# Kernel tuning notes

Hardware: AMD Instinct MI355X
Metric: run time of the kernel (lower is better)

Reference implementation:

```python
import jax, jax.numpy as jnp
import numpy as np

N_TAPS = 2
N_DELAY = 1
N_ITER = 3
EPS_MODEL = 1e-5   # LaplaceModel clamp eps (eps_models['laplace'])
EPS = 1e-3         # ISS divide/clamp eps


def mag_sq(x):
    return jnp.real(x) ** 2 + jnp.imag(x) ** 2


def laplace_weights(X):
    # Laplace source model: w[..., c, n] = 1 / (2 * ||X[..., c, :, n]||_2), broadcast over freq
    # X: (..., c, f, n) complex -> weights: (..., c, 1, n) real
    denom = 2.0 * jnp.sqrt(jnp.sum(mag_sq(X), axis=-2, keepdims=True))
    return 1.0 / jnp.maximum(denom, EPS_MODEL)


def iss_type1(src, Xc, weights):
    # Equation (9): update vector for source `src`
    Xs = Xc[..., src, :, :]  # (..., f, n)
    v_num = jnp.mean(weights * Xc * jnp.conj(Xs)[..., None, :, :], axis=-1)  # (..., c, f)
    v_denom = jnp.mean(weights * mag_sq(Xs)[..., None, :, :], axis=-1)       # (..., c, f) real
    v = v_num / jnp.maximum(v_denom, EPS)
    v_s = 1.0 - 1.0 / jnp.sqrt(jnp.maximum(v_denom[..., src, :], EPS))
    v = v.at[..., src, :].set(v_s.astype(v.dtype))
    return v


def iss_type2(src, tap, Xc, X_bar, weights):
    # update vector for dereverberation tap (src, tap)
    Xst = X_bar[..., src, :, tap, :]  # (..., f, n)
    v_num = jnp.mean(weights * Xc * jnp.conj(Xst)[..., None, :, :], axis=-1)
    # NOTE: the source code does NOT apply the 1/n_frames norm to v_denom here
    v_denom = jnp.sum(weights * mag_sq(Xst)[..., None, :, :], axis=-1)
    return v_num / jnp.maximum(v_denom, EPS)


def epoch_update(Xloc, Xc, W, X_bar, n_chan):
    weights = laplace_weights(Xloc)  # (..., c, 1, n)
    g = jnp.maximum(jnp.mean(mag_sq(Xloc), axis=(-2, -1), keepdims=True), 1e-5)
    Xloc = Xloc / jnp.sqrt(g)
    weights = weights * g
    for src in range(n_chan):
        v = iss_type1(src, Xc, weights)  # (..., c, f)
        Xc = Xc - v[..., None] * Xc[..., src, :, :][..., None, :, :]
        W = W - v[..., None] * W[..., src, :, :][..., None, :, :]
    for src in range(n_chan):
        for tap in range(N_TAPS):
            v = iss_type2(src, tap, Xc, X_bar, weights)
            Xc = Xc - v[..., None] * X_bar[..., src, :, tap, :][..., None, :, :]
    return Xloc, Xc, W


def auxiva_t_iss(X):
    batch = X.shape[:-3]
    n_chan, n_freq, n_frames = X.shape[-3:]
    T, D = N_TAPS, N_DELAY
    # hankel view of left-padded signal; keep only the T oldest rows (delayed taps)
    X_pad = jnp.pad(X, [(0, 0)] * (X.ndim - 1) + [(T + D, 0)])
    # X_bar: (..., c, f, T, n), X_bar[..., tap, t] = X[..., t - (T + D) + tap]
    X_bar = jnp.stack([X_pad[..., t:t + n_frames] for t in range(T)], axis=-2)
    eye = jnp.eye(n_chan, dtype=X.dtype)
    W = jnp.broadcast_to(eye[:, None, :], batch + (n_chan, n_freq, n_chan))
    Xloc = X  # the (buggy-but-faithful) local X that only gets renormalized each epoch
    Xc = X    # self.X, the demixed signal updated by ISS
    for _ in range(N_ITER):
        Xloc, Xc, W = epoch_update(Xloc, Xc, W, X_bar, n_chan)
    # projection back: a_f = (W_f^T)^{-1} e1 per frequency
    WT = jnp.swapaxes(jnp.swapaxes(W, -3, -2), -2, -1)  # (..., f, c, c)
    e1 = jnp.zeros((n_chan, 1), dtype=X.dtype).at[0, 0].set(1.0)
    a = jnp.linalg.solve(WT, e1)       # (..., f, c, 1)
    a = jnp.swapaxes(a, -3, -2)        # (..., c, f, 1)
    return Xc * a


def setup_inputs() -> dict:
    key = jax.random.key(0)
    k1, k2 = jax.random.split(key)
    shape = (4, 4, 257, 1024)  # (batch, n_chan, n_freq, n_frames)
    X_real = jax.random.normal(k1, shape, dtype=jnp.float32)
    X_imag = jax.random.normal(k2, shape, dtype=jnp.float32)
    return {"X_real": X_real, "X_imag": X_imag}


def reference(X_real, X_imag):
    X = jax.lax.complex(X_real, X_imag)
    return auxiva_t_iss(X)
```

## Files before the change

kernel.cpp:

```cpp
#include <hip/hip_runtime.h>
#include <math.h>

#define NB 4
#define NC 4
#define NF 257
#define NFR 1024
#define NTOT (NB * NC * NF * NFR)
#define NBC (NB * NC)
#define EPSV 1e-3f
#define EPS_MODEL 1e-5f
#define NCHUNK 32

typedef float v2f __attribute__((ext_vector_type(2)));

__device__ float g_Spart[NCHUNK * NBC * NFR];
__device__ float g_S[NBC * NFR];
__device__ float g_gP[96];

__device__ __forceinline__ float dpp_red_sum(float v) {
  v += __int_as_float(__builtin_amdgcn_update_dpp(0, __float_as_int(v), 0x111, 0xf, 0xf, true));
  v += __int_as_float(__builtin_amdgcn_update_dpp(0, __float_as_int(v), 0x112, 0xf, 0xf, true));
  v += __int_as_float(__builtin_amdgcn_update_dpp(0, __float_as_int(v), 0x114, 0xf, 0xf, true));
  v += __int_as_float(__builtin_amdgcn_update_dpp(0, __float_as_int(v), 0x118, 0xf, 0xf, true));
  v += __int_as_float(__builtin_amdgcn_update_dpp(0, __float_as_int(v), 0x142, 0xa, 0xf, true));
  v += __int_as_float(__builtin_amdgcn_update_dpp(0, __float_as_int(v), 0x143, 0xc, 0xf, true));
  return v;
}

__global__ __launch_bounds__(256) void k_colsum(const float* __restrict__ Xr,
                                                const float* __restrict__ Xi) {
  int u = blockIdx.x * 256 + threadIdx.x;
  int fc = blockIdx.y;
  int f0 = fc * 9;
  int f1 = f0 + 9; if (f1 > NF) f1 = NF;
  int bc = u >> 8, q = u & 255;
  float4 s = make_float4(0.f, 0.f, 0.f, 0.f);
  for (int f = f0; f < f1; ++f) {
    float4 a = reinterpret_cast<const float4*>(Xr + (bc * NF + f) * NFR)[q];
    float4 b = reinterpret_cast<const float4*>(Xi + (bc * NF + f) * NFR)[q];
    s.x += a.x * a.x + b.x * b.x;
    s.y += a.y * a.y + b.y * b.y;
    s.z += a.z * a.z + b.z * b.z;
    s.w += a.w * a.w + b.w * b.w;
  }
  reinterpret_cast<float4*>(g_Spart + fc * (NBC * NFR) + bc * NFR)[q] = s;
}

__global__ __launch_bounds__(256) void k_redgp() {
  int bc = blockIdx.x, tid = threadIdx.x;
  float4 s = make_float4(0.f, 0.f, 0.f, 0.f);
#pragma unroll
  for (int fc = 0; fc < NCHUNK; ++fc) {
    float4 a = reinterpret_cast<const float4*>(g_Spart + fc * (NBC * NFR) + bc * NFR)[tid];
    s.x += a.x; s.y += a.y; s.z += a.z; s.w += a.w;
  }
  reinterpret_cast<float4*>(g_S + bc * NFR)[tid] = s;
  float p = dpp_red_sum(s.x + s.y + s.z + s.w);
  __shared__ float r[4];
  if ((tid & 63) == 63) r[tid >> 6] = p;
  __syncthreads();
  if (tid == 0) {
    float s0 = (r[0] + r[1] + r[2] + r[3]) / (float)(NF * NFR);
    float P = 1.f;
#pragma unroll
    for (int e = 0; e < 3; ++e) {
      float g = fmaxf(s0 / P, 1e-5f);
      g_gP[e * 32 + bc] = g;
      g_gP[e * 32 + 16 + bc] = P;
      P *= g;
    }
  }
}

__device__ __forceinline__ void block_reduce12(float* __restrict__ p,
                                               float (*red)[2][12], int buf,
                                               int lane, int wvid,
                                               float* __restrict__ s) {
#pragma unroll
  for (int k = 0; k < 12; ++k) p[k] = dpp_red_sum(p[k]);
  if (lane == 63) {
    float4* dst = reinterpret_cast<float4*>(&red[buf][wvid][0]);
    dst[0] = make_float4(p[0], p[1], p[2], p[3]);
    dst[1] = make_float4(p[4], p[5], p[6], p[7]);
    dst[2] = make_float4(p[8], p[9], p[10], p[11]);
  }
  __syncthreads();
  const float4* r = reinterpret_cast<const float4*>(&red[buf][0][0]);
#pragma unroll
  for (int k = 0; k < 3; ++k) {
    float4 a = r[k], b = r[3 + k];
    s[4 * k + 0] = a.x + b.x;
    s[4 * k + 1] = a.y + b.y;
    s[4 * k + 2] = a.z + b.z;
    s[4 * k + 3] = a.w + b.w;
  }
}

__global__ __launch_bounds__(128, 2) void k_main(const float* __restrict__ Xr,
                                                 const float* __restrict__ Xi,
                                                 float* __restrict__ out, int nout) {
  const int blk = blockIdx.x;
  const int b = blk / NF, f = blk % NF;
  const int tid = threadIdx.x;
  const int lane = tid & 63, wvid = tid >> 6;
  const float invN = 1.f / (float)NFR;

  __shared__ float red[2][2][12];
  __shared__ float Wre[NC][NC], Wim[NC][NC];
  __shared__ float abc[8];

  v2f xcr[NC][4], xci[NC][4];
  int rowbase[NC];
#pragma unroll
  for (int c = 0; c < NC; ++c) {
    rowbase[c] = ((b * NC + c) * NF + f) * NFR;
    const float4* pr = reinterpret_cast<const float4*>(Xr + rowbase[c]);
    const float4* pi = reinterpret_cast<const float4*>(Xi + rowbase[c]);
    float4 a0 = pr[2 * tid], a1 = pr[2 * tid + 1];
    float4 b0 = pi[2 * tid], b1 = pi[2 * tid + 1];
    xcr[c][0] = (v2f){a0.x, a0.y}; xcr[c][1] = (v2f){a0.z, a0.w};
    xcr[c][2] = (v2f){a1.x, a1.y}; xcr[c][3] = (v2f){a1.z, a1.w};
    xci[c][0] = (v2f){b0.x, b0.y}; xci[c][1] = (v2f){b0.z, b0.w};
    xci[c][2] = (v2f){b1.x, b1.y}; xci[c][3] = (v2f){b1.z, b1.w};
  }
  if (tid < 16) {
    Wre[tid >> 2][tid & 3] = ((tid >> 2) == (tid & 3)) ? 1.f : 0.f;
    Wim[tid >> 2][tid & 3] = 0.f;
  }

  v2f w2[NC][4];
  int buf = 0;

  for (int e = 0; e < 3; ++e) {
#pragma unroll
    for (int c = 0; c < NC; ++c) {
      float g = g_gP[e * 32 + b * NC + c];
      float P = g_gP[e * 32 + 16 + b * NC + c];
      float sc = __builtin_amdgcn_rcpf(P);
      const float4* ps = reinterpret_cast<const float4*>(g_S + (b * NC + c) * NFR);
      float4 S0 = ps[2 * tid], S1 = ps[2 * tid + 1];
      float sv[8] = {S0.x, S0.y, S0.z, S0.w, S1.x, S1.y, S1.z, S1.w};
      float wv[8];
#pragma unroll
      for (int j = 0; j < 8; ++j)
        wv[j] = g * __builtin_amdgcn_rcpf(fmaxf(2.f * __builtin_amdgcn_sqrtf(sv[j] * sc), EPS_MODEL));
#pragma unroll
      for (int h = 0; h < 4; ++h) w2[c][h] = (v2f){wv[2 * h], wv[2 * h + 1]};
    }

    for (int src = 0; src < NC; ++src) {
      v2f p2[12];
#pragma unroll
      for (int k = 0; k < 12; ++k) p2[k] = (v2f){0.f, 0.f};
#pragma unroll
      for (int h = 0; h < 4; ++h) {
        v2f xsr = xcr[src][h], xsi = xci[src][h];
        v2f msq = xsr * xsr + xsi * xsi;
#pragma unroll
        for (int c = 0; c < NC; ++c) {
          v2f wv = w2[c][h];
          p2[c]     += wv * (xcr[c][h] * xsr + xci[c][h] * xsi);
          p2[4 + c] += wv * (xci[c][h] * xsr - xcr[c][h] * xsi);
          p2[8 + c] += wv * msq;
        }
      }
      float p[12];
#pragma unroll
      for (int k = 0; k < 12; ++k) p[k] = p2[k].x + p2[k].y;
      float s12[12];
      block_reduce12(p, red, buf, lane, wvid, s12);
      buf ^= 1;

      float vr[NC], vi[NC];
#pragma unroll
      for (int c = 0; c < NC; ++c) {
        float den = fmaxf(s12[8 + c] * invN, EPSV);
        if (c == src) {
          vr[c] = 1.f - __builtin_amdgcn_rsqf(den);
          vi[c] = 0.f;
        } else {
          float sc = invN * __builtin_amdgcn_rcpf(den);
          vr[c] = s12[c] * sc;
          vi[c] = s12[4 + c] * sc;
        }
      }
#pragma unroll
      for (int h = 0; h < 4; ++h) {
        v2f xsr = xcr[src][h], xsi = xci[src][h];
#pragma unroll
        for (int c = 0; c < NC; ++c) {
          xcr[c][h] -= xsr * vr[c] - xsi * vi[c];
          xci[c][h] -= xsi * vr[c] + xsr * vi[c];
        }
      }
      if (tid == 0) {
#pragma unroll
        for (int jj = 0; jj < NC; ++jj) {
          float wsr = Wre[src][jj], wsi = Wim[src][jj];
#pragma unroll
          for (int c = 0; c < NC; ++c) {
            Wre[c][jj] -= vr[c] * wsr - vi[c] * wsi;
            Wim[c][jj] -= vr[c] * wsi + vi[c] * wsr;
          }
        }
      }
    }

    for (int src = 0; src < NC; ++src) {
      const float4* pr = reinterpret_cast<const float4*>(Xr + rowbase[src]);
      const float4* pi = reinterpret_cast<const float4*>(Xi + rowbase[src]);
      float4 A4r = make_float4(0.f, 0.f, 0.f, 0.f), A4i = A4r;
      if (tid > 0) { A4r = pr[2 * tid - 1]; A4i = pi[2 * tid - 1]; }
      float4 B4r = pr[2 * tid], B4i = pi[2 * tid];
      float4 C4r = pr[2 * tid + 1], C4i = pi[2 * tid + 1];
      float wr[9] = {A4r.y, A4r.z, A4r.w, B4r.x, B4r.y, B4r.z, B4r.w, C4r.x, C4r.y};
      float wi[9] = {A4i.y, A4i.z, A4i.w, B4i.x, B4i.y, B4i.z, B4i.w, C4i.x, C4i.y};
      for (int tap = 0; tap < 2; ++tap) {
        v2f xs_r[4], xs_i[4];
#pragma unroll
        for (int h = 0; h < 4; ++h) {
          xs_r[h] = (v2f){wr[tap + 2 * h], wr[tap + 2 * h + 1]};
          xs_i[h] = (v2f){wi[tap + 2 * h], wi[tap + 2 * h + 1]};
        }
        v2f p2[12];
#pragma unroll
        for (int k = 0; k < 12; ++k) p2[k] = (v2f){0.f, 0.f};
#pragma unroll
        for (int h = 0; h < 4; ++h) {
          v2f xsr = xs_r[h], xsi = xs_i[h];
          v2f msq = xsr * xsr + xsi * xsi;
#pragma unroll
          for (int c = 0; c < NC; ++c) {
            v2f wv = w2[c][h];
            p2[c]     += wv * (xcr[c][h] * xsr + xci[c][h] * xsi);
            p2[4 + c] += wv * (xci[c][h] * xsr - xcr[c][h] * xsi);
            p2[8 + c] += wv * msq;
          }
        }
        float p[12];
#pragma unroll
        for (int k = 0; k < 12; ++k) p[k] = p2[k].x + p2[k].y;
        float s12[12];
        block_reduce12(p, red, buf, lane, wvid, s12);
        buf ^= 1;

        float vr[NC], vi[NC];
#pragma unroll
        for (int c = 0; c < NC; ++c) {
          float den = fmaxf(s12[8 + c], EPSV);
          float sc = invN * __builtin_amdgcn_rcpf(den);
          vr[c] = s12[c] * sc;
          vi[c] = s12[4 + c] * sc;
        }
#pragma unroll
        for (int h = 0; h < 4; ++h) {
          v2f xsr = xs_r[h], xsi = xs_i[h];
#pragma unroll
          for (int c = 0; c < NC; ++c) {
            xcr[c][h] -= xsr * vr[c] - xsi * vi[c];
            xci[c][h] -= xsi * vr[c] + xsr * vi[c];
          }
        }
      }
    }
  }

  __syncthreads();
  if (tid == 0) {
    float Ar[4][4], Ai[4][4];
    float br[4] = {1.f, 0.f, 0.f, 0.f}, bi[4] = {0.f, 0.f, 0.f, 0.f};
#pragma unroll
    for (int i = 0; i < 4; ++i)
#pragma unroll
      for (int j = 0; j < 4; ++j) {
        Ar[i][j] = Wre[j][i];
        Ai[i][j] = Wim[j][i];
      }
    for (int k = 0; k < 4; ++k) {
      int piv = k;
      float best = Ar[k][k] * Ar[k][k] + Ai[k][k] * Ai[k][k];
      for (int i = k + 1; i < 4; ++i) {
        float m = Ar[i][k] * Ar[i][k] + Ai[i][k] * Ai[i][k];
        if (m > best) { best = m; piv = i; }
      }
      if (piv != k) {
        for (int j = 0; j < 4; ++j) {
          float t = Ar[k][j]; Ar[k][j] = Ar[piv][j]; Ar[piv][j] = t;
          t = Ai[k][j]; Ai[k][j] = Ai[piv][j]; Ai[piv][j] = t;
        }
        float t = br[k]; br[k] = br[piv]; br[piv] = t;
        t = bi[k]; bi[k] = bi[piv]; bi[piv] = t;
      }
      float dr = Ar[k][k], di = Ai[k][k];
      float inv = 1.f / (dr * dr + di * di);
      for (int i = k + 1; i < 4; ++i) {
        float fr = (Ar[i][k] * dr + Ai[i][k] * di) * inv;
        float fi = (Ai[i][k] * dr - Ar[i][k] * di) * inv;
        for (int j = k; j < 4; ++j) {
          Ar[i][j] -= fr * Ar[k][j] - fi * Ai[k][j];
          Ai[i][j] -= fr * Ai[k][j] + fi * Ar[k][j];
        }
        br[i] -= fr * br[k] - fi * bi[k];
        bi[i] -= fr * bi[k] + fi * br[k];
      }
    }
    float ar[4], ai[4];
    for (int k = 3; k >= 0; --k) {
      float sr = br[k], si = bi[k];
      for (int j = k + 1; j < 4; ++j) {
        sr -= Ar[k][j] * ar[j] - Ai[k][j] * ai[j];
        si -= Ar[k][j] * ai[j] + Ai[k][j] * ar[j];
      }
      float dr = Ar[k][k], di = Ai[k][k];
      float inv = 1.f / (dr * dr + di * di);
      ar[k] = (sr * dr + si * di) * inv;
      ai[k] = (si * dr - sr * di) * inv;
    }
#pragma unroll
    for (int c = 0; c < 4; ++c) { abc[c] = ar[c]; abc[4 + c] = ai[c]; }
  }
  __syncthreads();

#pragma unroll
  for (int c = 0; c < NC; ++c) {
    float ar = abc[c], ai2 = abc[4 + c];
    if (rowbase[c] + 8 * tid + 7 < nout) {
      float4* po = reinterpret_cast<float4*>(out + rowbase[c]);
      v2f o0 = xcr[c][0] * ar - xci[c][0] * ai2;
      v2f o1 = xcr[c][1] * ar - xci[c][1] * ai2;
      v2f o2 = xcr[c][2] * ar - xci[c][2] * ai2;
      v2f o3 = xcr[c][3] * ar - xci[c][3] * ai2;
      po[2 * tid]     = make_float4(o0.x, o0.y, o1.x, o1.y);
      po[2 * tid + 1] = make_float4(o2.x, o2.y, o3.x, o3.y);
    }
  }
}

extern "C" void kernel_launch(void* const* d_in, const int* in_sizes, int n_in,
                              void* d_out, int out_size, void* d_ws, size_t ws_size,
                              hipStream_t stream) {
  const float* Xr = (const float*)d_in[0];
  const float* Xi = (const float*)d_in[1];
  float* out = (float*)d_out;

  dim3 g1(16, NCHUNK);
  k_colsum<<<g1, 256, 0, stream>>>(Xr, Xi);
  k_redgp<<<16, 256, 0, stream>>>();
  k_main<<<NB * NF, 128, 0, stream>>>(Xr, Xi, out, out_size);
}
```

Before: 194.7 us.

## Batch ISS updates via weighted Gram matrices to cut block reductions

Type-1 ISS now computes one weighted Hermitian Gram matrix per channel across all sources in a single block reduction. It then applies the four sequential source updates algebraically in registers, tracking the changes as a 4x4 mixing matrix applied to Xc and W once. Type-2 updates for both taps are fused into one reduction, with the cross term used to correct the second tap's numerator. This is meant to remove most of the per-source and per-tap reduction barriers and data passes, at the cost of more registers, larger reductions and small numerical differences from the reordered arithmetic.

```diff
diff --git a/kernel.cpp b/kernel.cpp
--- a/kernel.cpp
+++ b/kernel.cpp
@@ -16,6 +16,10 @@
 __device__ float g_Spart[NCHUNK * NBC * NFR];
 __device__ float g_S[NBC * NFR];
 __device__ float g_gP[96];
+
+__host__ __device__ constexpr int PIDX(int s, int t) {
+  return 3 * s - (s * (s - 1)) / 2 + (t - s - 1);
+}
 
 __device__ __forceinline__ float dpp_red_sum(float v) {
   v += __int_as_float(__builtin_amdgcn_update_dpp(0, __float_as_int(v), 0x111, 0xf, 0xf, true));
@@ -72,27 +76,27 @@
   }
 }
 
-__device__ __forceinline__ void block_reduce12(float* __restrict__ p,
-                                               float (*red)[2][12], int buf,
-                                               int lane, int wvid,
-                                               float* __restrict__ s) {
-#pragma unroll
-  for (int k = 0; k < 12; ++k) p[k] = dpp_red_sum(p[k]);
+template <int N>
+__device__ __forceinline__ void block_reduceN(float* p, float (*red)[2][64],
+                                              int buf, int lane, int wvid) {
+#pragma unroll
+  for (int k = 0; k < N; ++k) p[k] = dpp_red_sum(p[k]);
   if (lane == 63) {
     float4* dst = reinterpret_cast<float4*>(&red[buf][wvid][0]);
-    dst[0] = make_float4(p[0], p[1], p[2], p[3]);
-    dst[1] = make_float4(p[4], p[5], p[6], p[7]);
-    dst[2] = make_float4(p[8], p[9], p[10], p[11]);
+#pragma unroll
+    for (int k = 0; k < N / 4; ++k)
+      dst[k] = make_float4(p[4 * k], p[4 * k + 1], p[4 * k + 2], p[4 * k + 3]);
   }
   __syncthreads();
-  const float4* r = reinterpret_cast<const float4*>(&red[buf][0][0]);
-#pragma unroll
-  for (int k = 0; k < 3; ++k) {
-    float4 a = r[k], b = r[3 + k];
-    s[4 * k + 0] = a.x + b.x;
-    s[4 * k + 1] = a.y + b.y;
-    s[4 * k + 2] = a.z + b.z;
-    s[4 * k + 3] = a.w + b.w;
+  const float4* r0 = reinterpret_cast<const float4*>(&red[buf][0][0]);
+  const float4* r1 = reinterpret_cast<const float4*>(&red[buf][1][0]);
+#pragma unroll
+  for (int k = 0; k < N / 4; ++k) {
+    float4 a = r0[k], b = r1[k];
+    p[4 * k + 0] = a.x + b.x;
+    p[4 * k + 1] = a.y + b.y;
+    p[4 * k + 2] = a.z + b.z;
+    p[4 * k + 3] = a.w + b.w;
   }
 }
 
@@ -105,7 +109,7 @@
   const int lane = tid & 63, wvid = tid >> 6;
   const float invN = 1.f / (float)NFR;
 
-  __shared__ float red[2][2][12];
+  __shared__ float red[2][2][64];
   __shared__ float Wre[NC][NC], Wim[NC][NC];
   __shared__ float abc[8];
 
@@ -148,61 +152,148 @@
       for (int h = 0; h < 4; ++h) w2[c][h] = (v2f){wv[2 * h], wv[2 * h + 1]};
     }
 
-    for (int src = 0; src < NC; ++src) {
-      v2f p2[12];
-#pragma unroll
-      for (int k = 0; k < 12; ++k) p2[k] = (v2f){0.f, 0.f};
+    {
+      float hs[64];
+#pragma unroll
+      for (int k = 0; k < 64; ++k) hs[k] = 0.f;
 #pragma unroll
       for (int h = 0; h < 4; ++h) {
-        v2f xsr = xcr[src][h], xsi = xci[src][h];
-        v2f msq = xsr * xsr + xsi * xsi;
-#pragma unroll
-        for (int c = 0; c < NC; ++c) {
-          v2f wv = w2[c][h];
-          p2[c]     += wv * (xcr[c][h] * xsr + xci[c][h] * xsi);
-          p2[4 + c] += wv * (xci[c][h] * xsr - xcr[c][h] * xsi);
-          p2[8 + c] += wv * msq;
-        }
-      }
-      float p[12];
-#pragma unroll
-      for (int k = 0; k < 12; ++k) p[k] = p2[k].x + p2[k].y;
-      float s12[12];
-      block_reduce12(p, red, buf, lane, wvid, s12);
+#pragma unroll
+        for (int half = 0; half < 2; ++half) {
+          float xr[4], xi[4], wv[4];
+#pragma unroll
+          for (int s = 0; s < 4; ++s) {
+            xr[s] = half ? xcr[s][h].y : xcr[s][h].x;
+            xi[s] = half ? xci[s][h].y : xci[s][h].x;
+            wv[s] = half ? w2[s][h].y : w2[s][h].x;
+          }
+          float Pd[4], Pr[6], Pi[6];
+#pragma unroll
+          for (int s = 0; s < 4; ++s) Pd[s] = xr[s] * xr[s] + xi[s] * xi[s];
+#pragma unroll
+          for (int s = 0; s < 4; ++s)
+#pragma unroll
+            for (int t = s + 1; t < 4; ++t) {
+              const int q = PIDX(s, t);
+              Pr[q] = xr[s] * xr[t] + xi[s] * xi[t];
+              Pi[q] = xi[s] * xr[t] - xr[s] * xi[t];
+            }
+#pragma unroll
+          for (int c = 0; c < 4; ++c) {
+#pragma unroll
+            for (int s = 0; s < 4; ++s) hs[c * 16 + s] += wv[c] * Pd[s];
+#pragma unroll
+            for (int q = 0; q < 6; ++q) {
+              hs[c * 16 + 4 + 2 * q]     += wv[c] * Pr[q];
+              hs[c * 16 + 4 + 2 * q + 1] += wv[c] * Pi[q];
+            }
+          }
+        }
+      }
+      block_reduceN<64>(hs, red, buf, lane, wvid);
       buf ^= 1;
 
-      float vr[NC], vi[NC];
-#pragma unroll
-      for (int c = 0; c < NC; ++c) {
-        float den = fmaxf(s12[8 + c] * invN, EPSV);
-        if (c == src) {
-          vr[c] = 1.f - __builtin_amdgcn_rsqf(den);
-          vi[c] = 0.f;
-        } else {
-          float sc = invN * __builtin_amdgcn_rcpf(den);
-          vr[c] = s12[c] * sc;
-          vi[c] = s12[4 + c] * sc;
-        }
-      }
+      float Mr[4][4], Mi[4][4];
+#pragma unroll
+      for (int i = 0; i < 4; ++i)
+#pragma unroll
+        for (int j = 0; j < 4; ++j) { Mr[i][j] = (i == j) ? 1.f : 0.f; Mi[i][j] = 0.f; }
+
+#pragma unroll
+      for (int src = 0; src < 4; ++src) {
+        float vr[4], vi[4];
+#pragma unroll
+        for (int c = 0; c < 4; ++c) {
+          float den = fmaxf(hs[c * 16 + src] * invN, EPSV);
+          if (c == src) {
+            vr[c] = 1.f - __builtin_amdgcn_rsqf(den);
+            vi[c] = 0.f;
+          } else {
+            float nr, ni;
+            if (c < src) { const int q = PIDX(c, src); nr = hs[c * 16 + 4 + 2 * q]; ni = hs[c * 16 + 4 + 2 * q + 1]; }
+            else         { const int q = PIDX(src, c); nr = hs[c * 16 + 4 + 2 * q]; ni = -hs[c * 16 + 4 + 2 * q + 1]; }
+            float sc = invN * __builtin_amdgcn_rcpf(den);
+            vr[c] = nr * sc; vi[c] = ni * sc;
+          }
+        }
+        float msr[4], msi[4];
+#pragma unroll
+        for (int j = 0; j < 4; ++j) { msr[j] = Mr[src][j]; msi[j] = Mi[src][j]; }
+#pragma unroll
+        for (int c = 0; c < 4; ++c)
+#pragma unroll
+          for (int j = 0; j < 4; ++j) {
+            Mr[c][j] -= vr[c] * msr[j] - vi[c] * msi[j];
+            Mi[c][j] -= vr[c] * msi[j] + vi[c] * msr[j];
+          }
+        if (src < 3) {
+#pragma unroll
+          for (int c = 0; c < 4; ++c) {
+            const float d = hs[c * 16 + src];
+            float colr[4], coli[4];
+#pragma unroll
+            for (int s = 0; s < 4; ++s) {
+              if (s == src)      { colr[s] = d; coli[s] = 0.f; }
+              else if (s < src)  { const int q = PIDX(s, src); colr[s] = hs[c * 16 + 4 + 2 * q]; coli[s] = hs[c * 16 + 4 + 2 * q + 1]; }
+              else               { const int q = PIDX(src, s); colr[s] = hs[c * 16 + 4 + 2 * q]; coli[s] = -hs[c * 16 + 4 + 2 * q + 1]; }
+            }
+#pragma unroll
+            for (int s = 0; s < 4; ++s)
+              hs[c * 16 + s] += -2.f * (vr[s] * colr[s] + vi[s] * coli[s])
+                                + (vr[s] * vr[s] + vi[s] * vi[s]) * d;
+#pragma unroll
+            for (int s = 0; s < 4; ++s)
+#pragma unroll
+              for (int t = s + 1; t < 4; ++t) {
+                const int q = PIDX(s, t);
+                float hr = hs[c * 16 + 4 + 2 * q], hi = hs[c * 16 + 4 + 2 * q + 1];
+                hr -= vr[t] * colr[s] + vi[t] * coli[s];
+                hi -= vr[t] * coli[s] - vi[t] * colr[s];
+                hr -= vr[s] * colr[t] + vi[s] * coli[t];
+                hi -= vi[s] * colr[t] - vr[s] * coli[t];
+                float prr = vr[s] * vr[t] + vi[s] * vi[t];
+                float pii = vi[s] * vr[t] - vr[s] * vi[t];
+                hr += prr * d; hi += pii * d;
+                hs[c * 16 + 4 + 2 * q] = hr; hs[c * 16 + 4 + 2 * q + 1] = hi;
+              }
+          }
+        }
+      }
+
 #pragma unroll
       for (int h = 0; h < 4; ++h) {
-        v2f xsr = xcr[src][h], xsi = xci[src][h];
-#pragma unroll
-        for (int c = 0; c < NC; ++c) {
-          xcr[c][h] -= xsr * vr[c] - xsi * vi[c];
-          xci[c][h] -= xsi * vr[c] + xsr * vi[c];
-        }
-      }
+        v2f nr[4], ni[4];
+#pragma unroll
+        for (int c = 0; c < 4; ++c) {
+          nr[c] = (v2f){0.f, 0.f}; ni[c] = (v2f){0.f, 0.f};
+#pragma unroll
+          for (int s = 0; s < 4; ++s) {
+            nr[c] += Mr[c][s] * xcr[s][h] - Mi[c][s] * xci[s][h];
+            ni[c] += Mr[c][s] * xci[s][h] + Mi[c][s] * xcr[s][h];
+          }
+        }
+#pragma unroll
+        for (int c = 0; c < 4; ++c) { xcr[c][h] = nr[c]; xci[c][h] = ni[c]; }
+      }
+
       if (tid == 0) {
-#pragma unroll
-        for (int jj = 0; jj < NC; ++jj) {
-          float wsr = Wre[src][jj], wsi = Wim[src][jj];
-#pragma unroll
-          for (int c = 0; c < NC; ++c) {
-            Wre[c][jj] -= vr[c] * wsr - vi[c] * wsi;
-            Wim[c][jj] -= vr[c] * wsi + vi[c] * wsr;
-          }
-        }
+        float nWr[4][4], nWi[4][4];
+#pragma unroll
+        for (int c = 0; c < 4; ++c)
+#pragma unroll
+          for (int j = 0; j < 4; ++j) {
+            float sr = 0.f, si = 0.f;
+#pragma unroll
+            for (int s = 0; s < 4; ++s) {
+              sr += Mr[c][s] * Wre[s][j] - Mi[c][s] * Wim[s][j];
+              si += Mr[c][s] * Wim[s][j] + Mi[c][s] * Wre[s][j];
+            }
+            nWr[c][j] = sr; nWi[c][j] = si;
+          }
+#pragma unroll
+        for (int c = 0; c < 4; ++c)
+#pragma unroll
+          for (int j = 0; j < 4; ++j) { Wre[c][j] = nWr[c][j]; Wim[c][j] = nWi[c][j]; }
       }
     }
 
@@ -215,51 +306,61 @@
       float4 C4r = pr[2 * tid + 1], C4i = pi[2 * tid + 1];
       float wr[9] = {A4r.y, A4r.z, A4r.w, B4r.x, B4r.y, B4r.z, B4r.w, C4r.x, C4r.y};
       float wi[9] = {A4i.y, A4i.z, A4i.w, B4i.x, B4i.y, B4i.z, B4i.w, C4i.x, C4i.y};
-      for (int tap = 0; tap < 2; ++tap) {
-        v2f xs_r[4], xs_i[4];
-#pragma unroll
-        for (int h = 0; h < 4; ++h) {
-          xs_r[h] = (v2f){wr[tap + 2 * h], wr[tap + 2 * h + 1]};
-          xs_i[h] = (v2f){wi[tap + 2 * h], wi[tap + 2 * h + 1]};
-        }
-        v2f p2[12];
-#pragma unroll
-        for (int k = 0; k < 12; ++k) p2[k] = (v2f){0.f, 0.f};
-#pragma unroll
-        for (int h = 0; h < 4; ++h) {
-          v2f xsr = xs_r[h], xsi = xs_i[h];
-          v2f msq = xsr * xsr + xsi * xsi;
-#pragma unroll
-          for (int c = 0; c < NC; ++c) {
-            v2f wv = w2[c][h];
-            p2[c]     += wv * (xcr[c][h] * xsr + xci[c][h] * xsi);
-            p2[4 + c] += wv * (xci[c][h] * xsr - xcr[c][h] * xsi);
-            p2[8 + c] += wv * msq;
-          }
-        }
-        float p[12];
-#pragma unroll
-        for (int k = 0; k < 12; ++k) p[k] = p2[k].x + p2[k].y;
-        float s12[12];
-        block_reduce12(p, red, buf, lane, wvid, s12);
-        buf ^= 1;
-
-        float vr[NC], vi[NC];
+
+      v2f a2[32];
+#pragma unroll
+      for (int k = 0; k < 32; ++k) a2[k] = (v2f){0.f, 0.f};
+#pragma unroll
+      for (int h = 0; h < 4; ++h) {
+        v2f y0r = (v2f){wr[2 * h], wr[2 * h + 1]};
+        v2f y0i = (v2f){wi[2 * h], wi[2 * h + 1]};
+        v2f y1r = (v2f){wr[2 * h + 1], wr[2 * h + 2]};
+        v2f y1i = (v2f){wi[2 * h + 1], wi[2 * h + 2]};
+        v2f m0 = y0r * y0r + y0i * y0i;
+        v2f m1 = y1r * y1r + y1i * y1i;
+        v2f zr = y0r * y1r + y0i * y1i;
+        v2f zi = y0i * y1r - y0r * y1i;
 #pragma unroll
         for (int c = 0; c < NC; ++c) {
-          float den = fmaxf(s12[8 + c], EPSV);
-          float sc = invN * __builtin_amdgcn_rcpf(den);
-          vr[c] = s12[c] * sc;
-          vi[c] = s12[4 + c] * sc;
-        }
-#pragma unroll
-        for (int h = 0; h < 4; ++h) {
-          v2f xsr = xs_r[h], xsi = xs_i[h];
-#pragma unroll
-          for (int c = 0; c < NC; ++c) {
-            xcr[c][h] -= xsr * vr[c] - xsi * vi[c];
-            xci[c][h] -= xsi * vr[c] + xsr * vi[c];
-          }
+          v2f wv = w2[c][h];
+          a2[c]      += wv * (xcr[c][h] * y0r + xci[c][h] * y0i);
+          a2[4 + c]  += wv * (xci[c][h] * y0r - xcr[c][h] * y0i);
+          a2[8 + c]  += wv * (xcr[c][h] * y1r + xci[c][h] * y1i);
+          a2[12 + c] += wv * (xci[c][h] * y1r - xcr[c][h] * y1i);
+          a2[16 + c] += wv * m0;
+          a2[20 + c] += wv * m1;
+          a2[24 + c] += wv * zr;
+          a2[28 + c] += wv * zi;
+        }
+      }
+      float p[32];
+#pragma unroll
+      for (int k = 0; k < 32; ++k) p[k] = a2[k].x + a2[k].y;
+      block_reduceN<32>(p, red, buf, lane, wvid);
+      buf ^= 1;
+
+      float v0r[4], v0i[4], v1r[4], v1i[4];
+#pragma unroll
+      for (int c = 0; c < NC; ++c) {
+        float sc0 = invN * __builtin_amdgcn_rcpf(fmaxf(p[16 + c], EPSV));
+        v0r[c] = p[c] * sc0;
+        v0i[c] = p[4 + c] * sc0;
+        float n1r = p[8 + c]  - (v0r[c] * p[24 + c] - v0i[c] * p[28 + c]);
+        float n1i = p[12 + c] - (v0r[c] * p[28 + c] + v0i[c] * p[24 + c]);
+        float sc1 = invN * __builtin_amdgcn_rcpf(fmaxf(p[20 + c], EPSV));
+        v1r[c] = n1r * sc1;
+        v1i[c] = n1i * sc1;
+      }
+#pragma unroll
+      for (int h = 0; h < 4; ++h) {
+        v2f y0r = (v2f){wr[2 * h], wr[2 * h + 1]};
+        v2f y0i = (v2f){wi[2 * h], wi[2 * h + 1]};
+        v2f y1r = (v2f){wr[2 * h + 1], wr[2 * h + 2]};
+        v2f y1i = (v2f){wi[2 * h + 1], wi[2 * h + 2]};
+#pragma unroll
+        for (int c = 0; c < NC; ++c) {
+          xcr[c][h] -= y0r * v0r[c] - y0i * v0i[c] + y1r * v1r[c] - y1i * v1i[c];
+          xci[c][h] -= y0i * v0r[c] + y0r * v0i[c] + y1i * v1r[c] + y1r * v1i[c];
         }
       }
     }
```

After: 288.0 us. +47.9%, slower.

## Pair sequential ISS updates algebraically to halve block reductions per epoch

Applied to the files above, without the earlier changes.

Merges each pair of consecutive ISS updates (type-1 sources 0/1 and 2/3, and the two dereverberation taps per source) into one pass. A single 32-value block reduction gathers the extra cross and magnitude terms, from which the second update vector is derived algebraically. This halves the number of block-wide reductions and __syncthreads barriers per epoch, at the cost of more accumulators per thread. Launch bounds drop to one block per SIMD to make room for the higher register pressure, with some risk of float rounding differences.

```diff
diff --git a/kernel.cpp b/kernel.cpp
--- a/kernel.cpp
+++ b/kernel.cpp
@@ -72,31 +72,204 @@
   }
 }
 
-__device__ __forceinline__ void block_reduce12(float* __restrict__ p,
-                                               float (*red)[2][12], int buf,
-                                               int lane, int wvid,
-                                               float* __restrict__ s) {
-#pragma unroll
-  for (int k = 0; k < 12; ++k) p[k] = dpp_red_sum(p[k]);
+__device__ __forceinline__ void block_reduce32(float* p, float (*red)[2][32],
+                                               int buf, int lane, int wvid) {
+#pragma unroll
+  for (int k = 0; k < 32; ++k) p[k] = dpp_red_sum(p[k]);
   if (lane == 63) {
     float4* dst = reinterpret_cast<float4*>(&red[buf][wvid][0]);
-    dst[0] = make_float4(p[0], p[1], p[2], p[3]);
-    dst[1] = make_float4(p[4], p[5], p[6], p[7]);
-    dst[2] = make_float4(p[8], p[9], p[10], p[11]);
+#pragma unroll
+    for (int k = 0; k < 8; ++k)
+      dst[k] = make_float4(p[4 * k], p[4 * k + 1], p[4 * k + 2], p[4 * k + 3]);
   }
   __syncthreads();
-  const float4* r = reinterpret_cast<const float4*>(&red[buf][0][0]);
-#pragma unroll
-  for (int k = 0; k < 3; ++k) {
-    float4 a = r[k], b = r[3 + k];
-    s[4 * k + 0] = a.x + b.x;
-    s[4 * k + 1] = a.y + b.y;
-    s[4 * k + 2] = a.z + b.z;
-    s[4 * k + 3] = a.w + b.w;
-  }
-}
-
-__global__ __launch_bounds__(128, 2) void k_main(const float* __restrict__ Xr,
+  const float4* r0 = reinterpret_cast<const float4*>(&red[buf][0][0]);
+  const float4* r1 = reinterpret_cast<const float4*>(&red[buf][1][0]);
+#pragma unroll
+  for (int k = 0; k < 8; ++k) {
+    float4 a = r0[k], b = r1[k];
+    p[4 * k + 0] = a.x + b.x;
+    p[4 * k + 1] = a.y + b.y;
+    p[4 * k + 2] = a.z + b.z;
+    p[4 * k + 3] = a.w + b.w;
+  }
+}
+
+template <int S0, int S1>
+__device__ __forceinline__ void t1_pair(v2f (&xcr)[NC][4], v2f (&xci)[NC][4],
+                                        v2f (&w2)[NC][4],
+                                        float (&Wre)[NC][NC], float (&Wim)[NC][NC],
+                                        float (*red)[2][32], int& buf,
+                                        int lane, int wvid, int tid, float invN) {
+  float p[32];
+#pragma unroll
+  for (int k = 0; k < 32; ++k) p[k] = 0.f;
+#pragma unroll
+  for (int h = 0; h < 4; ++h) {
+    v2f y0r = xcr[S0][h], y0i = xci[S0][h];
+    v2f y1r = xcr[S1][h], y1i = xci[S1][h];
+    v2f m0 = y0r * y0r + y0i * y0i;
+    v2f m1 = y1r * y1r + y1i * y1i;
+    v2f zr = y0r * y1r + y0i * y1i;
+    v2f zi = y0i * y1r - y0r * y1i;
+#pragma unroll
+    for (int c = 0; c < NC; ++c) {
+      v2f wv = w2[c][h];
+      v2f t;
+      t = xcr[c][h] * y0r + xci[c][h] * y0i;  p[c]      += wv.x * t.x + wv.y * t.y;
+      t = xci[c][h] * y0r - xcr[c][h] * y0i;  p[4 + c]  += wv.x * t.x + wv.y * t.y;
+      t = xcr[c][h] * y1r + xci[c][h] * y1i;  p[8 + c]  += wv.x * t.x + wv.y * t.y;
+      t = xci[c][h] * y1r - xcr[c][h] * y1i;  p[12 + c] += wv.x * t.x + wv.y * t.y;
+      p[16 + c] += wv.x * m0.x + wv.y * m0.y;
+      p[20 + c] += wv.x * m1.x + wv.y * m1.y;
+      p[24 + c] += wv.x * zr.x + wv.y * zr.y;
+      p[28 + c] += wv.x * zi.x + wv.y * zi.y;
+    }
+  }
+  block_reduce32(p, red, buf, lane, wvid);
+  buf ^= 1;
+
+  float v0r[4], v0i[4];
+#pragma unroll
+  for (int c = 0; c < 4; ++c) {
+    float den = fmaxf(p[16 + c] * invN, EPSV);
+    if (c == S0) {
+      v0r[c] = 1.f - __builtin_amdgcn_rsqf(den);
+      v0i[c] = 0.f;
+    } else {
+      float sc = invN * __builtin_amdgcn_rcpf(den);
+      v0r[c] = p[c] * sc;
+      v0i[c] = p[4 + c] * sc;
+    }
+  }
+  const float ar = v0r[S1], ai = v0i[S1];
+  const float amag = ar * ar + ai * ai;
+
+  float v1r[4], v1i[4];
+#pragma unroll
+  for (int c = 0; c < 4; ++c) {
+    float den1 = p[20 + c] - 2.f * (ar * p[24 + c] - ai * p[28 + c]) + amag * p[16 + c];
+    float den = fmaxf(den1 * invN, EPSV);
+    if (c == S1) {
+      v1r[c] = 1.f - __builtin_amdgcn_rsqf(den);
+      v1i[c] = 0.f;
+    } else {
+      float nr = p[8 + c]  - (ar * p[c] + ai * p[4 + c])
+                 - (v0r[c] * p[24 + c] - v0i[c] * p[28 + c])
+                 + (v0r[c] * ar + v0i[c] * ai) * p[16 + c];
+      float ni = p[12 + c] - (ar * p[4 + c] - ai * p[c])
+                 - (v0r[c] * p[28 + c] + v0i[c] * p[24 + c])
+                 + (v0i[c] * ar - v0r[c] * ai) * p[16 + c];
+      float sc = invN * __builtin_amdgcn_rcpf(den);
+      v1r[c] = nr * sc;
+      v1i[c] = ni * sc;
+    }
+  }
+
+  float u0r[4], u0i[4];
+#pragma unroll
+  for (int c = 0; c < 4; ++c) {
+    u0r[c] = v0r[c] - (v1r[c] * ar - v1i[c] * ai);
+    u0i[c] = v0i[c] - (v1r[c] * ai + v1i[c] * ar);
+  }
+
+#pragma unroll
+  for (int h = 0; h < 4; ++h) {
+    v2f y0r = xcr[S0][h], y0i = xci[S0][h];
+    v2f y1r = xcr[S1][h], y1i = xci[S1][h];
+#pragma unroll
+    for (int c = 0; c < NC; ++c) {
+      xcr[c][h] -= y0r * u0r[c] - y0i * u0i[c] + y1r * v1r[c] - y1i * v1i[c];
+      xci[c][h] -= y0i * u0r[c] + y0r * u0i[c] + y1i * v1r[c] + y1r * v1i[c];
+    }
+  }
+
+  if (tid == 0) {
+#pragma unroll
+    for (int j = 0; j < NC; ++j) {
+      float w0r = Wre[S0][j], w0i = Wim[S0][j];
+      float w1r = Wre[S1][j], w1i = Wim[S1][j];
+#pragma unroll
+      for (int c = 0; c < NC; ++c) {
+        Wre[c][j] -= u0r[c] * w0r - u0i[c] * w0i + v1r[c] * w1r - v1i[c] * w1i;
+        Wim[c][j] -= u0r[c] * w0i + u0i[c] * w0r + v1r[c] * w1i + v1i[c] * w1r;
+      }
+    }
+  }
+}
+
+__device__ __forceinline__ void t2_stage(const float* __restrict__ prb,
+                                         const float* __restrict__ pib,
+                                         v2f (&xcr)[NC][4], v2f (&xci)[NC][4],
+                                         v2f (&w2)[NC][4],
+                                         float (*red)[2][32], int& buf,
+                                         int lane, int wvid, int tid, float invN) {
+  const float4* pr = reinterpret_cast<const float4*>(prb);
+  const float4* pi = reinterpret_cast<const float4*>(pib);
+  float4 A4r = make_float4(0.f, 0.f, 0.f, 0.f), A4i = A4r;
+  if (tid > 0) { A4r = pr[2 * tid - 1]; A4i = pi[2 * tid - 1]; }
+  float4 B4r = pr[2 * tid], B4i = pi[2 * tid];
+  float4 C4r = pr[2 * tid + 1], C4i = pi[2 * tid + 1];
+  float wr[9] = {A4r.y, A4r.z, A4r.w, B4r.x, B4r.y, B4r.z, B4r.w, C4r.x, C4r.y};
+  float wi[9] = {A4i.y, A4i.z, A4i.w, B4i.x, B4i.y, B4i.z, B4i.w, C4i.x, C4i.y};
+
+  float p[32];
+#pragma unroll
+  for (int k = 0; k < 32; ++k) p[k] = 0.f;
+#pragma unroll
+  for (int h = 0; h < 4; ++h) {
+    v2f y0r = (v2f){wr[2 * h], wr[2 * h + 1]};
+    v2f y0i = (v2f){wi[2 * h], wi[2 * h + 1]};
+    v2f y1r = (v2f){wr[2 * h + 1], wr[2 * h + 2]};
+    v2f y1i = (v2f){wi[2 * h + 1], wi[2 * h + 2]};
+    v2f m0 = y0r * y0r + y0i * y0i;
+    v2f m1 = y1r * y1r + y1i * y1i;
+    v2f zr = y0r * y1r + y0i * y1i;
+    v2f zi = y0i * y1r - y0r * y1i;
+#pragma unroll
+    for (int c = 0; c < NC; ++c) {
+      v2f wv = w2[c][h];
+      v2f t;
+      t = xcr[c][h] * y0r + xci[c][h] * y0i;  p[c]      += wv.x * t.x + wv.y * t.y;
+      t = xci[c][h] * y0r - xcr[c][h] * y0i;  p[4 + c]  += wv.x * t.x + wv.y * t.y;
+      t = xcr[c][h] * y1r + xci[c][h] * y1i;  p[8 + c]  += wv.x * t.x + wv.y * t.y;
+      t = xci[c][h] * y1r - xcr[c][h] * y1i;  p[12 + c] += wv.x * t.x + wv.y * t.y;
+      p[16 + c] += wv.x * m0.x + wv.y * m0.y;
+      p[20 + c] += wv.x * m1.x + wv.y * m1.y;
+      p[24 + c] += wv.x * zr.x + wv.y * zr.y;
+      p[28 + c] += wv.x * zi.x + wv.y * zi.y;
+    }
+  }
+  block_reduce32(p, red, buf, lane, wvid);
+  buf ^= 1;
+
+  float v0r[4], v0i[4], v1r[4], v1i[4];
+#pragma unroll
+  for (int c = 0; c < NC; ++c) {
+    float sc0 = invN * __builtin_amdgcn_rcpf(fmaxf(p[16 + c], EPSV));
+    v0r[c] = p[c] * sc0;
+    v0i[c] = p[4 + c] * sc0;
+    float n1r = p[8 + c]  - (v0r[c] * p[24 + c] - v0i[c] * p[28 + c]);
+    float n1i = p[12 + c] - (v0r[c] * p[28 + c] + v0i[c] * p[24 + c]);
+    float sc1 = invN * __builtin_amdgcn_rcpf(fmaxf(p[20 + c], EPSV));
+    v1r[c] = n1r * sc1;
+    v1i[c] = n1i * sc1;
+  }
+#pragma unroll
+  for (int h = 0; h < 4; ++h) {
+    v2f y0r = (v2f){wr[2 * h], wr[2 * h + 1]};
+    v2f y0i = (v2f){wi[2 * h], wi[2 * h + 1]};
+    v2f y1r = (v2f){wr[2 * h + 1], wr[2 * h + 2]};
+    v2f y1i = (v2f){wi[2 * h + 1], wi[2 * h + 2]};
+#pragma unroll
+    for (int c = 0; c < NC; ++c) {
+      xcr[c][h] -= y0r * v0r[c] - y0i * v0i[c] + y1r * v1r[c] - y1i * v1i[c];
+      xci[c][h] -= y0i * v0r[c] + y0r * v0i[c] + y1i * v1r[c] + y1r * v1i[c];
+    }
+  }
+}
+
+__global__ __launch_bounds__(128, 1) void k_main(const float* __restrict__ Xr,
                                                  const float* __restrict__ Xi,
                                                  float* __restrict__ out, int nout) {
   const int blk = blockIdx.x;
@@ -105,7 +278,7 @@
   const int lane = tid & 63, wvid = tid >> 6;
   const float invN = 1.f / (float)NFR;
 
-  __shared__ float red[2][2][12];
+  __shared__ float red[2][2][32];
   __shared__ float Wre[NC][NC], Wim[NC][NC];
   __shared__ float abc[8];
 
@@ -148,121 +321,13 @@
       for (int h = 0; h < 4; ++h) w2[c][h] = (v2f){wv[2 * h], wv[2 * h + 1]};
     }
 
-    for (int src = 0; src < NC; ++src) {
-      v2f p2[12];
-#pragma unroll
-      for (int k = 0; k < 12; ++k) p2[k] = (v2f){0.f, 0.f};
-#pragma unroll
-      for (int h = 0; h < 4; ++h) {
-        v2f xsr = xcr[src][h], xsi = xci[src][h];
-        v2f msq = xsr * xsr + xsi * xsi;
-#pragma unroll
-        for (int c = 0; c < NC; ++c) {
-          v2f wv = w2[c][h];
-          p2[c]     += wv * (xcr[c][h] * xsr + xci[c][h] * xsi);
-          p2[4 + c] += wv * (xci[c][h] * xsr - xcr[c][h] * xsi);
-          p2[8 + c] += wv * msq;
-        }
-      }
-      float p[12];
-#pragma unroll
-      for (int k = 0; k < 12; ++k) p[k] = p2[k].x + p2[k].y;
-      float s12[12];
-      block_reduce12(p, red, buf, lane, wvid, s12);
-      buf ^= 1;
-
-      float vr[NC], vi[NC];
-#pragma unroll
-      for (int c = 0; c < NC; ++c) {
-        float den = fmaxf(s12[8 + c] * invN, EPSV);
-        if (c == src) {
-          vr[c] = 1.f - __builtin_amdgcn_rsqf(den);
-          vi[c] = 0.f;
-        } else {
-          float sc = invN * __builtin_amdgcn_rcpf(den);
-          vr[c] = s12[c] * sc;
-          vi[c] = s12[4 + c] * sc;
-        }
-      }
-#pragma unroll
-      for (int h = 0; h < 4; ++h) {
-        v2f xsr = xcr[src][h], xsi = xci[src][h];
-#pragma unroll
-        for (int c = 0; c < NC; ++c) {
-          xcr[c][h] -= xsr * vr[c] - xsi * vi[c];
-          xci[c][h] -= xsi * vr[c] + xsr * vi[c];
-        }
-      }
-      if (tid == 0) {
-#pragma unroll
-        for (int jj = 0; jj < NC; ++jj) {
-          float wsr = Wre[src][jj], wsi = Wim[src][jj];
-#pragma unroll
-          for (int c = 0; c < NC; ++c) {
-            Wre[c][jj] -= vr[c] * wsr - vi[c] * wsi;
-            Wim[c][jj] -= vr[c] * wsi + vi[c] * wsr;
-          }
-        }
-      }
-    }
-
-    for (int src = 0; src < NC; ++src) {
-      const float4* pr = reinterpret_cast<const float4*>(Xr + rowbase[src]);
-      const float4* pi = reinterpret_cast<const float4*>(Xi + rowbase[src]);
-      float4 A4r = make_float4(0.f, 0.f, 0.f, 0.f), A4i = A4r;
-      if (tid > 0) { A4r = pr[2 * tid - 1]; A4i = pi[2 * tid - 1]; }
-      float4 B4r = pr[2 * tid], B4i = pi[2 * tid];
-      float4 C4r = pr[2 * tid + 1], C4i = pi[2 * tid + 1];
-      float wr[9] = {A4r.y, A4r.z, A4r.w, B4r.x, B4r.y, B4r.z, B4r.w, C4r.x, C4r.y};
-      float wi[9] = {A4i.y, A4i.z, A4i.w, B4i.x, B4i.y, B4i.z, B4i.w, C4i.x, C4i.y};
-      for (int tap = 0; tap < 2; ++tap) {
-        v2f xs_r[4], xs_i[4];
-#pragma unroll
-        for (int h = 0; h < 4; ++h) {
-          xs_r[h] = (v2f){wr[tap + 2 * h], wr[tap + 2 * h + 1]};
-          xs_i[h] = (v2f){wi[tap + 2 * h], wi[tap + 2 * h + 1]};
-        }
-        v2f p2[12];
-#pragma unroll
-        for (int k = 0; k < 12; ++k) p2[k] = (v2f){0.f, 0.f};
-#pragma unroll
-        for (int h = 0; h < 4; ++h) {
-          v2f xsr = xs_r[h], xsi = xs_i[h];
-          v2f msq = xsr * xsr + xsi * xsi;
-#pragma unroll
-          for (int c = 0; c < NC; ++c) {
-            v2f wv = w2[c][h];
-            p2[c]     += wv * (xcr[c][h] * xsr + xci[c][h] * xsi);
-            p2[4 + c] += wv * (xci[c][h] * xsr - xcr[c][h] * xsi);
-            p2[8 + c] += wv * msq;
-          }
-        }
-        float p[12];
-#pragma unroll
-        for (int k = 0; k < 12; ++k) p[k] = p2[k].x + p2[k].y;
-        float s12[12];
-        block_reduce12(p, red, buf, lane, wvid, s12);
-        buf ^= 1;
-
-        float vr[NC], vi[NC];
-#pragma unroll
-        for (int c = 0; c < NC; ++c) {
-          float den = fmaxf(s12[8 + c], EPSV);
-          float sc = invN * __builtin_amdgcn_rcpf(den);
-          vr[c] = s12[c] * sc;
-          vi[c] = s12[4 + c] * sc;
-        }
-#pragma unroll
-        for (int h = 0; h < 4; ++h) {
-          v2f xsr = xs_r[h], xsi = xs_i[h];
-#pragma unroll
-          for (int c = 0; c < NC; ++c) {
-            xcr[c][h] -= xsr * vr[c] - xsi * vi[c];
-            xci[c][h] -= xsi * vr[c] + xsr * vi[c];
-          }
-        }
-      }
-    }
+    t1_pair<0, 1>(xcr, xci, w2, Wre, Wim, red, buf, lane, wvid, tid, invN);
+    t1_pair<2, 3>(xcr, xci, w2, Wre, Wim, red, buf, lane, wvid, tid, invN);
+
+    t2_stage(Xr + rowbase[0], Xi + rowbase[0], xcr, xci, w2, red, buf, lane, wvid, tid, invN);
+    t2_stage(Xr + rowbase[1], Xi + rowbase[1], xcr, xci, w2, red, buf, lane, wvid, tid, invN);
+    t2_stage(Xr + rowbase[2], Xi + rowbase[2], xcr, xci, w2, red, buf, lane, wvid, tid, invN);
+    t2_stage(Xr + rowbase[3], Xi + rowbase[3], xcr, xci, w2, red, buf, lane, wvid, tid, invN);
   }
 
   __syncthreads();
```

Result: slower. 257.9 us (+32.5%).
